# Optimization experiments

Measured on AMD Instinct MI355X. Metric: run time of the kernel, lower is better.

Reference implementation:

```python
import jax, jax.numpy as jnp
import numpy as np

B, S, D_IN, D_H, D_LAT, D_OUT = 128, 1024, 64, 256, 256, 128
N_PIECES = 20
NEG_BIG = -99999.0


def setup_inputs() -> dict:
    key = jax.random.key(0)
    ks = jax.random.split(key, 12)
    def lin(k, fan_in, fan_out):
        bound = 1.0 / np.sqrt(fan_in)
        kw, kb = jax.random.split(k)
        w = jax.random.uniform(kw, (fan_in, fan_out), minval=-bound, maxval=bound, dtype=jnp.float32)
        b = jax.random.uniform(kb, (fan_out,), minval=-bound, maxval=bound, dtype=jnp.float32)
        return w, b
    x = jax.random.normal(ks[0], (B, S, D_IN), dtype=jnp.float32)
    mask = jax.random.randint(ks[1], (B, S, 1), 0, 2, dtype=jnp.int32)
    phi_w1, phi_b1 = lin(ks[2], D_IN, D_H)
    phi_w2, phi_b2 = lin(ks[3], D_H, D_LAT)
    rho_w1, rho_b1 = lin(ks[4], D_LAT, D_H)
    rho_w2, rho_b2 = lin(ks[5], D_H, D_OUT)
    pool_w = 0.1 * jax.random.normal(ks[6], (D_LAT, N_PIECES + 1), dtype=jnp.float32)
    return dict(x=x, mask=mask, phi_w1=phi_w1, phi_b1=phi_b1, phi_w2=phi_w2, phi_b2=phi_b2,
                rho_w1=rho_w1, rho_b1=rho_b1, rho_w2=rho_w2, rho_b2=rho_b2, pool_w=pool_w)


def _fspool(x, n, w):
    # x: [B, C, S] features per channel over set dim; n: [B] ragged sizes; w: [C, P+1]
    b, c, s = x.shape
    # positions mapped to [0,1] ratio of the (n-1)-long valid prefix (fill_sizes)
    ratio = jnp.arange(s, dtype=jnp.float32)[None, :] / jnp.maximum(n.astype(jnp.float32) - 1.0, 1.0)[:, None]  # [B,S]
    m = (ratio <= 1.0).astype(x.dtype)          # [B,S], first n positions valid
    ratio = jnp.minimum(ratio, 1.0)
    # piecewise-linear interpolation of continuous weight function (determine_weight)
    pos = N_PIECES * ratio                       # [B,S]
    idx = jnp.floor(pos).astype(jnp.int32)
    frac = (pos - idx)[:, None, :]               # [B,1,S]
    left = jnp.take(w, idx, axis=1).transpose(1, 0, 2)                                   # [B,C,S]
    right = jnp.take(w, jnp.clip(idx + 1, 0, N_PIECES), axis=1).transpose(1, 0, 2)       # [B,C,S]
    weight = (1.0 - frac) * left + frac * right  # [B,C,S]
    # push padded entries to the bottom, sort descending per channel
    xm = x + (1.0 - m)[:, None, :] * NEG_BIG
    xs = jnp.flip(jnp.sort(xm, axis=2), axis=2)  # descending
    return jnp.sum(xs * weight * m[:, None, :], axis=2)  # [B,C]


def reference(x, mask, phi_w1, phi_b1, phi_w2, phi_b2, rho_w1, rho_b1, rho_w2, rho_b2, pool_w):
    # phi per-element MLP: [B,S,d_in] -> [B,S,d_lat]
    h = jax.nn.relu(jnp.einsum('bsi,ih->bsh', x, phi_w1) + phi_b1)
    feat = jnp.einsum('bsh,hl->bsl', h, phi_w2) + phi_b2
    feat = jnp.transpose(feat, (0, 2, 1))        # [B, d_lat, S]
    n = jnp.sum(mask, axis=1).squeeze(-1)        # [B]
    pooled = _fspool(feat, n, pool_w)            # [B, d_lat]
    # rho MLP
    h2 = jax.nn.relu(pooled @ rho_w1 + rho_b1)
    return h2 @ rho_w2 + rho_b2                  # [B, d_out]
```

## Files before the change

### kernel.cpp

```cpp
#include <hip/hip_runtime.h>
#include <hip/hip_bf16.h>

#define B_    128
#define S_    1024
#define DIN   64
#define DH    256
#define DLAT  256
#define DOUT  128
#define NPIECES 20

typedef short bf16x8 __attribute__((ext_vector_type(8)));
typedef float f32x4  __attribute__((ext_vector_type(4)));
typedef unsigned short u16x2 __attribute__((ext_vector_type(2)));

__device__ __forceinline__ unsigned short f2b(float f) {
    union { float f; unsigned u; } a; a.f = f;
    unsigned r = a.u + 0x7fffu + ((a.u >> 16) & 1u);
    return (unsigned short)(r >> 16);
}
__device__ __forceinline__ float b2f_u(unsigned u16bits) {
    union { unsigned u; float f; } a; a.u = u16bits << 16;
    return a.f;
}
__device__ __forceinline__ unsigned pmaxu(unsigned a, unsigned b) {
    union { unsigned u; u16x2 v; } A, Bv, R;
    A.u = a; Bv.u = b;
    R.v = __builtin_elementwise_max(A.v, Bv.v);
    return R.u;
}
__device__ __forceinline__ unsigned pminu(unsigned a, unsigned b) {
    union { unsigned u; u16x2 v; } A, Bv, R;
    A.u = a; Bv.u = b;
    R.v = __builtin_elementwise_min(A.v, Bv.v);
    return R.u;
}
__device__ __forceinline__ unsigned ror16(unsigned x) { return (x >> 16) | (x << 16); }

__device__ __forceinline__ bf16x8 cvt8(float4 a, float4 b) {
    bf16x8 o;
    o[0] = (short)f2b(a.x); o[1] = (short)f2b(a.y); o[2] = (short)f2b(a.z); o[3] = (short)f2b(a.w);
    o[4] = (short)f2b(b.x); o[5] = (short)f2b(b.y); o[6] = (short)f2b(b.z); o[7] = (short)f2b(b.w);
    return o;
}

__global__ __launch_bounds__(256) void k_prep(const int* __restrict__ mask,
                                              int* __restrict__ nv,
                                              const float* __restrict__ w1,
                                              short* __restrict__ w1pk,
                                              const float* __restrict__ w2,
                                              short* __restrict__ w2pk) {
    __shared__ int parts[4];
    const int blk = blockIdx.x, t = threadIdx.x;
    if (blk < B_) {
        int sum = 0;
        #pragma unroll
        for (int q = 0; q < S_ / 256; ++q) sum += mask[blk * S_ + q * 256 + t];
        #pragma unroll
        for (int off = 32; off > 0; off >>= 1) sum += __shfl_down(sum, off, 64);
        if ((t & 63) == 0) parts[t >> 6] = sum;
        __syncthreads();
        if (t == 0) nv[blk] = max(parts[0] + parts[1] + parts[2] + parts[3], 2);
    } else if (blk < B_ + 8) {
        int c = (blk - B_) * 256 + t;
        int l = c & 63, ks = (c >> 6) % 2, nt = (c >> 6) / 2;
        int col = nt * 16 + (l & 15);
        int k0 = ks * 32 + (l >> 4) * 8;
        bf16x8 o;
        #pragma unroll
        for (int j = 0; j < 8; ++j) o[j] = (short)f2b(w1[(size_t)(k0 + j) * DH + col]);
        *(bf16x8*)(w1pk + (size_t)c * 8) = o;
    } else {
        int c = (blk - B_ - 8) * 256 + t;
        int l = c & 63, ks = (c >> 6) % 8, nt = (c >> 6) / 8;
        int col = nt * 16 + (l & 15);
        int k0 = ks * 32 + (l >> 4) * 8;
        bf16x8 o;
        #pragma unroll
        for (int j = 0; j < 8; ++j) o[j] = (short)f2b(w2[(size_t)(k0 + j) * DLAT + col]);
        *(bf16x8*)(w2pk + (size_t)c * 8) = o;
    }
}

__global__ __launch_bounds__(256) void k_phi_mfma(const float* __restrict__ x,
                                                  const short* __restrict__ w1pk,
                                                  const short* __restrict__ w2pk,
                                                  const float* __restrict__ b1,
                                                  const float* __restrict__ b2,
                                                  const int* __restrict__ nv,
                                                  unsigned short* __restrict__ feat) {
    const int b    = blockIdx.y;
    const int tile = blockIdx.x;
    const int s0   = tile * 64;
    if (s0 >= nv[b]) return;
    const int tid  = threadIdx.x;
    const int w    = tid >> 6;
    const int lane = tid & 63;
    const int c15  = lane & 15;
    const int q    = lane >> 4;

    __shared__ __align__(16) char lds[64 * 256 * 2];

    f32x4 acc1[4][4];
    #pragma unroll
    for (int mt = 0; mt < 4; ++mt)
        #pragma unroll
        for (int nt = 0; nt < 4; ++nt) acc1[mt][nt] = (f32x4)0.f;

    const float* xb = x + ((size_t)b * S_ + s0) * DIN;
    bf16x8 a1[4][2], bw[4][2];
    #pragma unroll
    for (int mt = 0; mt < 4; ++mt)
        #pragma unroll
        for (int ks = 0; ks < 2; ++ks) {
            const float* p = xb + (size_t)(mt * 16 + c15) * DIN + ks * 32 + q * 8;
            float4 v0 = *(const float4*)p;
            float4 v1 = *(const float4*)(p + 4);
            a1[mt][ks] = cvt8(v0, v1);
        }
    #pragma unroll
    for (int nt = 0; nt < 4; ++nt)
        #pragma unroll
        for (int ks = 0; ks < 2; ++ks)
            bw[nt][ks] = *(const bf16x8*)(w1pk + ((size_t)((w * 4 + nt) * 2 + ks) * 64 + lane) * 8);
    #pragma unroll
    for (int ks = 0; ks < 2; ++ks)
        #pragma unroll
        for (int mt = 0; mt < 4; ++mt)
            #pragma unroll
            for (int nt = 0; nt < 4; ++nt)
                acc1[mt][nt] = __builtin_amdgcn_mfma_f32_16x16x32_bf16(a1[mt][ks], bw[nt][ks], acc1[mt][nt], 0, 0, 0);

    #pragma unroll
    for (int nt = 0; nt < 4; ++nt) {
        int chan = (w * 4 + nt) * 16 + c15;
        float bias = b1[chan];
        #pragma unroll
        for (int mt = 0; mt < 4; ++mt)
            #pragma unroll
            for (int r = 0; r < 4; ++r) {
                int pos = mt * 16 + q * 4 + r;
                float hv = fmaxf(acc1[mt][nt][r] + bias, 0.f);
                int byte = pos * 512 + chan * 2;
                byte ^= (pos & 7) << 4;
                *(unsigned short*)(lds + byte) = f2b(hv);
            }
    }
    __syncthreads();

    f32x4 acc2[4][4];
    #pragma unroll
    for (int mt = 0; mt < 4; ++mt)
        #pragma unroll
        for (int nt = 0; nt < 4; ++nt) acc2[mt][nt] = (f32x4)0.f;

    for (int ks2 = 0; ks2 < 8; ++ks2) {
        bf16x8 af[4];
        #pragma unroll
        for (int mt = 0; mt < 4; ++mt) {
            int pos = mt * 16 + c15;
            int byte = pos * 512 + ks2 * 64 + q * 16;
            byte ^= (pos & 7) << 4;
            af[mt] = *(const bf16x8*)(lds + byte);
        }
        #pragma unroll
        for (int nt = 0; nt < 4; ++nt) {
            bf16x8 bf_ = *(const bf16x8*)(w2pk + ((size_t)((w * 4 + nt) * 8 + ks2) * 64 + lane) * 8);
            #pragma unroll
            for (int mt = 0; mt < 4; ++mt)
                acc2[mt][nt] = __builtin_amdgcn_mfma_f32_16x16x32_bf16(af[mt], bf_, acc2[mt][nt], 0, 0, 0);
        }
    }
    __syncthreads();

    #pragma unroll
    for (int nt = 0; nt < 4; ++nt) {
        int chan = (w * 4 + nt) * 16 + c15;
        float bias = b2[chan];
        #pragma unroll
        for (int mt = 0; mt < 4; ++mt) {
            unsigned u0 = (unsigned)f2b(acc2[mt][nt][0] + bias) | ((unsigned)f2b(acc2[mt][nt][1] + bias) << 16);
            unsigned u1 = (unsigned)f2b(acc2[mt][nt][2] + bias) | ((unsigned)f2b(acc2[mt][nt][3] + bias) << 16);
            int pos0 = mt * 16 + q * 4;
            int byte = chan * 128 + pos0 * 2;
            byte ^= (chan & 7) << 4;
            *(uint2*)(lds + byte) = uint2{u0, u1};
        }
    }
    __syncthreads();

    #pragma unroll
    for (int it = 0; it < 8; ++it) {
        int L = it * 256 + tid;
        int chan = L >> 3, chunk = L & 7;
        int byte = chan * 128 + chunk * 16;
        byte ^= (chan & 7) << 4;
        uint4 val = *(const uint4*)(lds + byte);
        *(uint4*)((char*)(feat + ((size_t)b * DLAT + chan) * S_ + s0) + chunk * 16) = val;
    }
}


template <int T0, int NREGS>
__device__ __forceinline__ void loadcvt4(const unsigned short* __restrict__ fp, int i0, int n,
                                         unsigned (&r)[NREGS]) {
    uint4 a = *(const uint4*)(fp + i0);
    r[T0 + 0] = a.x; r[T0 + 1] = a.y; r[T0 + 2] = a.z; r[T0 + 3] = a.w;
    #pragma unroll
    for (int t = 0; t < 4; ++t) {
        unsigned u = r[T0 + t];
        unsigned sgn = (u >> 15) & 0x00010001u;
        unsigned key = u ^ ((sgn * 0x7FFFu) | 0x80008000u);
        int e0 = i0 + 2 * t;
        unsigned keep = (e0 + 1 < n) ? 0xFFFFFFFFu : ((e0 < n) ? 0x0000FFFFu : 0u);
        r[T0 + t] = key & keep;
    }
}

template <int T0, int NREGS>
__device__ __forceinline__ void pass_cross(unsigned (&r)[NREGS], int lane, int m, int k) {
    bool lower = ((lane & m) == 0);
    bool dz = (((lane << 3) & k) == 0);
    bool sel = (dz == lower);
    #pragma unroll
    for (int t = 0; t < 4; ++t) {
        unsigned p = __shfl_xor(r[T0 + t], m, 64);
        unsigned mx = pmaxu(r[T0 + t], p), mn = pminu(r[T0 + t], p);
        r[T0 + t] = sel ? mx : mn;
    }
}

template <int T0, int NREGS>
__device__ __forceinline__ void pass_pair(unsigned (&r)[NREGS], int lane, int jr, int k) {
    #pragma unroll
    for (int t = 0; t < 4; ++t)
        if ((t & jr) == 0) {
            int ta = T0 + t, tb = T0 + (t | jr);
            unsigned mx = pmaxu(r[ta], r[tb]), mn = pminu(r[ta], r[tb]);
            bool dz = ((((lane << 3) | (t << 1)) & k) == 0);
            r[ta] = dz ? mx : mn;
            r[tb] = dz ? mn : mx;
        }
}

template <int T0, int NREGS>
__device__ __forceinline__ void pass_inpack(unsigned (&r)[NREGS], int lane, int k) {
    #pragma unroll
    for (int t = 0; t < 4; ++t) {
        unsigned v = r[T0 + t];
        unsigned sw = ror16(v);
        unsigned mx = pmaxu(v, sw), mn = pminu(v, sw);
        bool dz = ((((lane << 3) | (t << 1)) & k) == 0);
        unsigned de = (mx & 0x0000FFFFu) | (mn & 0xFFFF0000u);
        unsigned as = (mn & 0x0000FFFFu) | (mx & 0xFFFF0000u);
        r[T0 + t] = dz ? de : as;
    }
}

template <int NET, int T0, int NREGS>
__device__ __forceinline__ void sort_net(unsigned (&r)[NREGS], int lane) {
    #pragma unroll
    for (int k = 2; k <= NET; k <<= 1) {
        #pragma unroll
        for (int j = k >> 1; j > 0; j >>= 1) {
            if (j >= 8)      pass_cross<T0>(r, lane, j >> 3, k);
            else if (j >= 2) pass_pair<T0>(r, lane, j >> 1, k);
            else             pass_inpack<T0>(r, lane, k);
        }
    }
}

__device__ __forceinline__ void merge_desc512_dual(unsigned (&r)[8], int lane) {
    #pragma unroll
    for (int j = 256; j >= 8; j >>= 1) {
        const int m = j >> 3;
        bool sel = ((lane & m) == 0);
        #pragma unroll
        for (int t = 0; t < 8; ++t) {
            unsigned p = __shfl_xor(r[t], m, 64);
            unsigned mx = pmaxu(r[t], p), mn = pminu(r[t], p);
            r[t] = sel ? mx : mn;
        }
    }
    #pragma unroll
    for (int jr = 2; jr >= 1; jr >>= 1)
        #pragma unroll
        for (int g = 0; g < 8; g += 4)
            #pragma unroll
            for (int t = 0; t < 4; ++t)
                if ((t & jr) == 0) {
                    unsigned a = r[g + t], bb = r[g + (t | jr)];
                    r[g + t]        = pmaxu(a, bb);
                    r[g + (t | jr)] = pminu(a, bb);
                }
    #pragma unroll
    for (int t = 0; t < 8; ++t) {
        unsigned sw = ror16(r[t]);
        unsigned mx = pmaxu(r[t], sw), mn = pminu(r[t], sw);
        r[t] = (mx & 0x0000FFFFu) | (mn & 0xFFFF0000u);
    }
}

template <bool FASTW, int T0, int NREGS>
__device__ __forceinline__ float wsum(const unsigned (&r)[NREGS], int rankBase, int n,
                                      float invd, const float* __restrict__ pw) {
    float acc = 0.f;
    float k0 = 0.f, k1 = 0.f, k2 = 0.f; int ib = 0;
    if (FASTW) {
        float rb = fminf((float)rankBase * invd, 1.0f);
        ib = (int)((float)NPIECES * rb);
        if (ib > NPIECES) ib = NPIECES;
        k0 = pw[ib]; k1 = pw[min(ib + 1, NPIECES)]; k2 = pw[min(ib + 2, NPIECES)];
    }
    #pragma unroll
    for (int t = 0; t < 4; ++t)
        #pragma unroll
        for (int h = 0; h < 2; ++h) {
            int i = rankBase + 2 * t + h;
            unsigned key = h ? (r[T0 + t] >> 16) : (r[T0 + t] & 0xFFFFu);
            unsigned tneg = ((key >> 15) & 1u) ^ 1u;
            unsigned u = key ^ (0x8000u | (tneg * 0x7FFFu));
            float v = (i < n) ? b2f_u(u) : 0.f;
            float ratio = fminf((float)i * invd, 1.0f);
            float pos = (float)NPIECES * ratio;
            int idx = (int)pos;
            float frac = pos - (float)idx;
            float L, R;
            if (FASTW) { L = (idx == ib) ? k0 : k1; R = (idx == ib) ? k1 : k2; }
            else       { L = pw[idx];  R = pw[min(idx + 1, NPIECES)]; }
            acc = fmaf(v, fmaf(frac, R - L, L), acc);
        }
    return acc;
}

__device__ __forceinline__ float fsp_sum16(const unsigned short* __restrict__ fp,
                                           int n, const float* __restrict__ pw, int lane) {
    const int base = lane * 16;
    unsigned r[8];
    {
        const uint4* q4 = (const uint4*)(fp + base);
        uint4 a = q4[0], bq = q4[1];
        r[0] = a.x;  r[1] = a.y;  r[2] = a.z;  r[3] = a.w;
        r[4] = bq.x; r[5] = bq.y; r[6] = bq.z; r[7] = bq.w;
    }
    #pragma unroll
    for (int t = 0; t < 8; ++t) {
        unsigned u = r[t];
        unsigned sgn = (u >> 15) & 0x00010001u;
        unsigned key = u ^ ((sgn * 0x7FFFu) | 0x80008000u);
        int i0 = base + 2 * t;
        unsigned keep = (i0 + 1 < n) ? 0xFFFFFFFFu : ((i0 < n) ? 0x0000FFFFu : 0u);
        r[t] = key & keep;
    }
    #pragma unroll
    for (int k = 2; k <= 1024; k <<= 1) {
        #pragma unroll
        for (int j = k >> 1; j > 0; j >>= 1) {
            if (j >= 16) {
                const int m = j >> 4;
                const bool dz  = (((lane * 16) & k) == 0);
                const bool sel = (dz == ((lane & m) == 0));
                #pragma unroll
                for (int t = 0; t < 8; ++t) {
                    unsigned p = __shfl_xor(r[t], m, 64);
                    unsigned mx = pmaxu(r[t], p), mn = pminu(r[t], p);
                    r[t] = sel ? mx : mn;
                }
            } else if (j >= 2) {
                const int jr = j >> 1;
                #pragma unroll
                for (int t = 0; t < 8; ++t)
                    if ((t & jr) == 0) {
                        const int tb = t | jr;
                        unsigned mx = pmaxu(r[t], r[tb]), mn = pminu(r[t], r[tb]);
                        const bool dz = ((((lane * 16) | (2 * t)) & k) == 0);
                        r[t]  = dz ? mx : mn;
                        r[tb] = dz ? mn : mx;
                    }
            } else {
                #pragma unroll
                for (int t = 0; t < 8; ++t) {
                    unsigned sw = ror16(r[t]);
                    unsigned mx = pmaxu(r[t], sw), mn = pminu(r[t], sw);
                    const bool dz = ((((lane * 16) | (2 * t)) & k) == 0);
                    unsigned de = (mx & 0x0000FFFFu) | (mn & 0xFFFF0000u);
                    unsigned as = (mn & 0x0000FFFFu) | (mx & 0xFFFF0000u);
                    r[t] = dz ? de : as;
                }
            }
        }
    }
    const float invd = 1.0f / (float)(n - 1);
    float acc = 0.f;
    float rb = fminf((float)base * invd, 1.0f);
    int ib = (int)((float)NPIECES * rb);
    if (ib > NPIECES) ib = NPIECES;
    float k0 = pw[ib], k1 = pw[min(ib + 1, NPIECES)], k2 = pw[min(ib + 2, NPIECES)];
    #pragma unroll
    for (int t = 0; t < 8; ++t)
        #pragma unroll
        for (int h = 0; h < 2; ++h) {
            int i = base + 2 * t + h;
            unsigned key = h ? (r[t] >> 16) : (r[t] & 0xFFFFu);
            unsigned tneg = ((key >> 15) & 1u) ^ 1u;
            unsigned u = key ^ (0x8000u | (tneg * 0x7FFFu));
            float v = (i < n) ? b2f_u(u) : 0.f;
            float ratio = fminf((float)i * invd, 1.0f);
            float pos = (float)NPIECES * ratio;
            int idx = (int)pos;
            float frac = pos - (float)idx;
            float L = (idx == ib) ? k0 : k1, R = (idx == ib) ? k1 : k2;
            acc = fmaf(v, fmaf(frac, R - L, L), acc);
        }
    return acc;
}

__global__ __launch_bounds__(256) void k_fspool4(const unsigned short* __restrict__ feat,
                                                 const int* __restrict__ nv,
                                                 const float* __restrict__ pool_w,
                                                 float* __restrict__ pooled) {
    const int gw   = blockIdx.x * 4 + (threadIdx.x >> 6);
    const int lane = threadIdx.x & 63;
    const int b = gw >> 8, c = gw & 255;
    const int n = nv[b];
    const unsigned short* fp = feat + ((size_t)b * DLAT + c) * S_;
    const float* pw = pool_w + c * (NPIECES + 1);
    const float invd = 1.0f / (float)(n - 1);

    float res;
    if (n <= 512) {
        unsigned r[4];
        loadcvt4<0>(fp, lane * 8, n, r);
        sort_net<512, 0>(r, lane);
        res = (n >= 141) ? wsum<true, 0>(r, lane * 8, n, invd, pw)
                         : wsum<false, 0>(r, lane * 8, n, invd, pw);
    } else if (n <= 640) {
        unsigned r[8];
        loadcvt4<0>(fp, lane * 8, n, r);
        loadcvt4<4>(fp, 512 + lane * 8, n, r);
        sort_net<512, 0>(r, lane);
        sort_net<128, 4>(r, lane);
        unsigned pa[4], pb[4];
        #pragma unroll
        for (int t = 0; t < 4; ++t) pa[t] = ror16(__shfl_xor(r[7 - t], 63, 64));
        #pragma unroll
        for (int t = 0; t < 4; ++t) pb[t] = ror16(__shfl_xor(r[3 - t], 63, 64));
        #pragma unroll
        for (int t = 0; t < 4; ++t) r[t]     = pmaxu(r[t], pa[t]);
        #pragma unroll
        for (int t = 0; t < 4; ++t) r[4 + t] = pminu(r[4 + t], pb[t]);
        merge_desc512_dual(r, lane);
        res = wsum<true, 0>(r, lane * 8, n, invd, pw)
            + wsum<true, 4>(r, 512 + lane * 8, n, invd, pw);
    } else {
        res = fsp_sum16(fp, n, pw, lane);
    }
    #pragma unroll
    for (int off = 32; off > 0; off >>= 1) res += __shfl_xor(res, off, 64);
    if (lane == 0) pooled[gw] = res;
}

__global__ __launch_bounds__(256) void k_rho(const float* __restrict__ pooled,
                                             const float* __restrict__ w1,
                                             const float* __restrict__ b1,
                                             const float* __restrict__ w2,
                                             const float* __restrict__ b2,
                                             float* __restrict__ out) {
    const int b = blockIdx.x, t = threadIdx.x;
    __shared__ float pl[DLAT];
    __shared__ float h2[DH];
    pl[t] = pooled[b * DLAT + t];
    __syncthreads();
    float acc = b1[t];
    for (int k = 0; k < DLAT; ++k) acc = fmaf(pl[k], w1[k * DH + t], acc);
    h2[t] = fmaxf(acc, 0.f);
    __syncthreads();
    if (t < DOUT) {
        float o = b2[t];
        for (int k = 0; k < DH; ++k) o = fmaf(h2[k], w2[k * DOUT + t], o);
        out[b * DOUT + t] = o;
    }
}

extern "C" void kernel_launch(void* const* d_in, const int* in_sizes, int n_in,
                              void* d_out, int out_size, void* d_ws, size_t ws_size,
                              hipStream_t stream) {
    const float* x     = (const float*)d_in[0];
    const int*   mask  = (const int*)d_in[1];
    const float* pw1   = (const float*)d_in[2];
    const float* pb1   = (const float*)d_in[3];
    const float* pw2   = (const float*)d_in[4];
    const float* pb2   = (const float*)d_in[5];
    const float* rw1   = (const float*)d_in[6];
    const float* rb1   = (const float*)d_in[7];
    const float* rw2   = (const float*)d_in[8];
    const float* rb2   = (const float*)d_in[9];
    const float* poolw = (const float*)d_in[10];
    float* out = (float*)d_out;

    char* ws = (char*)d_ws;
    size_t off = 0;
    int* nv = (int*)ws;                          off += 1024;
    short* w1pk  = (short*)(ws + off);           off += (size_t)DIN * DH * 2;
    short* w2pk  = (short*)(ws + off);           off += (size_t)DH * DLAT * 2;
    unsigned short* feat = (unsigned short*)(ws + off); off += (size_t)B_ * DLAT * S_ * 2;
    float* pooled = (float*)(ws + off);

    k_prep<<<B_ + 8 + 32, 256, 0, stream>>>(mask, nv, pw1, w1pk, pw2, w2pk);
    k_phi_mfma<<<dim3(S_ / 64, B_), 256, 0, stream>>>(x, w1pk, w2pk, pb1, pb2, nv, feat);
    k_fspool4<<<(B_ * DLAT) / 4, 256, 0, stream>>>(feat, nv, poolw, pooled);
    k_rho<<<B_, 256, 0, stream>>>(pooled, rw1, rb1, rw2, rb2, out);
}
```

Before: 132.8 us.

## Roll bitonic sort stages into loops and unify large-n path via two 512-sorts plus merge

Replaces the fully unrolled bitonic sort networks with partially rolled loops over stage k and cross-lane distance j, and hardcodes the first in-register stages. The separate 16-element-per-lane path for n>640 is removed; that case now reuses the two-half 512 sort plus dual merge. Byte-permute instructions replace the mask/or packing of min/max halves. The intent is to cut instruction-cache footprint and code size, and to share one code path across all set sizes, at the cost of loop overhead and runtime-indexed shuffles.

```diff
diff --git a/kernel.cpp b/kernel.cpp
--- a/kernel.cpp
+++ b/kernel.cpp
@@ -35,6 +35,13 @@
     return R.u;
 }
 __device__ __forceinline__ unsigned ror16(unsigned x) { return (x >> 16) | (x << 16); }
+__device__ __forceinline__ unsigned permb(unsigned a, unsigned b, unsigned s) {
+    return __builtin_amdgcn_perm(a, b, s);
+}
+__device__ __forceinline__ unsigned keycvt(unsigned u) {
+    unsigned sgn = (u >> 15) & 0x00010001u;
+    return u ^ ((sgn * 0x7FFFu) | 0x80008000u);
+}
 
 __device__ __forceinline__ bf16x8 cvt8(float4 a, float4 b) {
     bf16x8 o;
@@ -207,9 +214,7 @@
     r[T0 + 0] = a.x; r[T0 + 1] = a.y; r[T0 + 2] = a.z; r[T0 + 3] = a.w;
     #pragma unroll
     for (int t = 0; t < 4; ++t) {
-        unsigned u = r[T0 + t];
-        unsigned sgn = (u >> 15) & 0x00010001u;
-        unsigned key = u ^ ((sgn * 0x7FFFu) | 0x80008000u);
+        unsigned key = keycvt(r[T0 + t]);
         int e0 = i0 + 2 * t;
         unsigned keep = (e0 + 1 < n) ? 0xFFFFFFFFu : ((e0 < n) ? 0x0000FFFFu : 0u);
         r[T0 + t] = key & keep;
@@ -217,86 +222,95 @@
 }
 
 template <int T0, int NREGS>
-__device__ __forceinline__ void pass_cross(unsigned (&r)[NREGS], int lane, int m, int k) {
-    bool lower = ((lane & m) == 0);
-    bool dz = (((lane << 3) & k) == 0);
-    bool sel = (dz == lower);
+__device__ __forceinline__ void sort512_loop(unsigned (&r)[NREGS], int lane, int kmax) {
     #pragma unroll
     for (int t = 0; t < 4; ++t) {
-        unsigned p = __shfl_xor(r[T0 + t], m, 64);
-        unsigned mx = pmaxu(r[T0 + t], p), mn = pminu(r[T0 + t], p);
-        r[T0 + t] = sel ? mx : mn;
-    }
-}
-
-template <int T0, int NREGS>
-__device__ __forceinline__ void pass_pair(unsigned (&r)[NREGS], int lane, int jr, int k) {
-    #pragma unroll
-    for (int t = 0; t < 4; ++t)
-        if ((t & jr) == 0) {
-            int ta = T0 + t, tb = T0 + (t | jr);
-            unsigned mx = pmaxu(r[ta], r[tb]), mn = pminu(r[ta], r[tb]);
-            bool dz = ((((lane << 3) | (t << 1)) & k) == 0);
-            r[ta] = dz ? mx : mn;
-            r[tb] = dz ? mn : mx;
-        }
-}
-
-template <int T0, int NREGS>
-__device__ __forceinline__ void pass_inpack(unsigned (&r)[NREGS], int lane, int k) {
+        unsigned v = r[T0 + t], sw = ror16(v);
+        unsigned mx = pmaxu(v, sw), mn = pminu(v, sw);
+        r[T0 + t] = ((t & 1) == 0) ? permb(mn, mx, 0x07060100u) : permb(mx, mn, 0x07060100u);
+    }
+    {
+        unsigned mx0 = pmaxu(r[T0 + 0], r[T0 + 1]), mn0 = pminu(r[T0 + 0], r[T0 + 1]);
+        r[T0 + 0] = mx0; r[T0 + 1] = mn0;
+        unsigned mx1 = pmaxu(r[T0 + 2], r[T0 + 3]), mn1 = pminu(r[T0 + 2], r[T0 + 3]);
+        r[T0 + 2] = mn1; r[T0 + 3] = mx1;
+    }
     #pragma unroll
     for (int t = 0; t < 4; ++t) {
-        unsigned v = r[T0 + t];
-        unsigned sw = ror16(v);
+        unsigned v = r[T0 + t], sw = ror16(v);
         unsigned mx = pmaxu(v, sw), mn = pminu(v, sw);
-        bool dz = ((((lane << 3) | (t << 1)) & k) == 0);
-        unsigned de = (mx & 0x0000FFFFu) | (mn & 0xFFFF0000u);
-        unsigned as = (mn & 0x0000FFFFu) | (mx & 0xFFFF0000u);
-        r[T0 + t] = dz ? de : as;
-    }
-}
-
-template <int NET, int T0, int NREGS>
-__device__ __forceinline__ void sort_net(unsigned (&r)[NREGS], int lane) {
-    #pragma unroll
-    for (int k = 2; k <= NET; k <<= 1) {
-        #pragma unroll
-        for (int j = k >> 1; j > 0; j >>= 1) {
-            if (j >= 8)      pass_cross<T0>(r, lane, j >> 3, k);
-            else if (j >= 2) pass_pair<T0>(r, lane, j >> 1, k);
-            else             pass_inpack<T0>(r, lane, k);
-        }
-    }
-}
-
-__device__ __forceinline__ void merge_desc512_dual(unsigned (&r)[8], int lane) {
-    #pragma unroll
+        r[T0 + t] = (t < 2) ? permb(mn, mx, 0x07060100u) : permb(mx, mn, 0x07060100u);
+    }
+    #pragma clang loop unroll(disable)
+    for (int k = 8; k <= kmax; k <<= 1) {
+        const bool dzk = (((lane << 3) & k) == 0);
+        #pragma clang loop unroll(disable)
+        for (int j = k >> 1; j >= 8; j >>= 1) {
+            const int m = j >> 3;
+            const bool sel = (dzk == ((lane & m) == 0));
+            #pragma unroll
+            for (int t = 0; t < 4; ++t) {
+                unsigned p = (unsigned)__shfl_xor((int)r[T0 + t], m, 64);
+                unsigned mx = pmaxu(r[T0 + t], p), mn = pminu(r[T0 + t], p);
+                r[T0 + t] = sel ? mx : mn;
+            }
+        }
+        #pragma unroll
+        for (int t = 0; t < 2; ++t) {
+            unsigned a = r[T0 + t], bb = r[T0 + t + 2];
+            unsigned mx = pmaxu(a, bb), mn = pminu(a, bb);
+            r[T0 + t]     = dzk ? mx : mn;
+            r[T0 + t + 2] = dzk ? mn : mx;
+        }
+        #pragma unroll
+        for (int t = 0; t < 4; t += 2) {
+            unsigned a = r[T0 + t], bb = r[T0 + t + 1];
+            unsigned mx = pmaxu(a, bb), mn = pminu(a, bb);
+            r[T0 + t]     = dzk ? mx : mn;
+            r[T0 + t + 1] = dzk ? mn : mx;
+        }
+        #pragma unroll
+        for (int t = 0; t < 4; ++t) {
+            unsigned v = r[T0 + t], sw = ror16(v);
+            unsigned mx = pmaxu(v, sw), mn = pminu(v, sw);
+            unsigned de = permb(mn, mx, 0x07060100u);
+            unsigned as = permb(mx, mn, 0x07060100u);
+            r[T0 + t] = dzk ? de : as;
+        }
+    }
+}
+
+__device__ __forceinline__ void merge512_dual_loop(unsigned (&r)[8], int lane) {
+    #pragma clang loop unroll(disable)
     for (int j = 256; j >= 8; j >>= 1) {
         const int m = j >> 3;
-        bool sel = ((lane & m) == 0);
+        const bool sel = ((lane & m) == 0);
         #pragma unroll
         for (int t = 0; t < 8; ++t) {
-            unsigned p = __shfl_xor(r[t], m, 64);
+            unsigned p = (unsigned)__shfl_xor((int)r[t], m, 64);
             unsigned mx = pmaxu(r[t], p), mn = pminu(r[t], p);
             r[t] = sel ? mx : mn;
         }
     }
     #pragma unroll
-    for (int jr = 2; jr >= 1; jr >>= 1)
-        #pragma unroll
-        for (int g = 0; g < 8; g += 4)
-            #pragma unroll
-            for (int t = 0; t < 4; ++t)
-                if ((t & jr) == 0) {
-                    unsigned a = r[g + t], bb = r[g + (t | jr)];
-                    r[g + t]        = pmaxu(a, bb);
-                    r[g + (t | jr)] = pminu(a, bb);
-                }
+    for (int g = 0; g < 8; g += 4) {
+        #pragma unroll
+        for (int t = 0; t < 2; ++t) {
+            unsigned a = r[g + t], bb = r[g + t + 2];
+            r[g + t]     = pmaxu(a, bb);
+            r[g + t + 2] = pminu(a, bb);
+        }
+        #pragma unroll
+        for (int t = 0; t < 4; t += 2) {
+            unsigned a = r[g + t], bb = r[g + t + 1];
+            r[g + t]     = pmaxu(a, bb);
+            r[g + t + 1] = pminu(a, bb);
+        }
+    }
     #pragma unroll
     for (int t = 0; t < 8; ++t) {
         unsigned sw = ror16(r[t]);
-        unsigned mx = pmaxu(r[t], sw), mn = pminu(r[t], sw);
-        r[t] = (mx & 0x0000FFFFu) | (mn & 0xFFFF0000u);
+        r[t] = permb(pminu(r[t], sw), pmaxu(r[t], sw), 0x07060100u);
     }
 }
 
@@ -332,92 +346,10 @@
     return acc;
 }
 
-__device__ __forceinline__ float fsp_sum16(const unsigned short* __restrict__ fp,
-                                           int n, const float* __restrict__ pw, int lane) {
-    const int base = lane * 16;
-    unsigned r[8];
-    {
-        const uint4* q4 = (const uint4*)(fp + base);
-        uint4 a = q4[0], bq = q4[1];
-        r[0] = a.x;  r[1] = a.y;  r[2] = a.z;  r[3] = a.w;
-        r[4] = bq.x; r[5] = bq.y; r[6] = bq.z; r[7] = bq.w;
-    }
-    #pragma unroll
-    for (int t = 0; t < 8; ++t) {
-        unsigned u = r[t];
-        unsigned sgn = (u >> 15) & 0x00010001u;
-        unsigned key = u ^ ((sgn * 0x7FFFu) | 0x80008000u);
-        int i0 = base + 2 * t;
-        unsigned keep = (i0 + 1 < n) ? 0xFFFFFFFFu : ((i0 < n) ? 0x0000FFFFu : 0u);
-        r[t] = key & keep;
-    }
-    #pragma unroll
-    for (int k = 2; k <= 1024; k <<= 1) {
-        #pragma unroll
-        for (int j = k >> 1; j > 0; j >>= 1) {
-            if (j >= 16) {
-                const int m = j >> 4;
-                const bool dz  = (((lane * 16) & k) == 0);
-                const bool sel = (dz == ((lane & m) == 0));
-                #pragma unroll
-                for (int t = 0; t < 8; ++t) {
-                    unsigned p = __shfl_xor(r[t], m, 64);
-                    unsigned mx = pmaxu(r[t], p), mn = pminu(r[t], p);
-                    r[t] = sel ? mx : mn;
-                }
-            } else if (j >= 2) {
-                const int jr = j >> 1;
-                #pragma unroll
-                for (int t = 0; t < 8; ++t)
-                    if ((t & jr) == 0) {
-                        const int tb = t | jr;
-                        unsigned mx = pmaxu(r[t], r[tb]), mn = pminu(r[t], r[tb]);
-                        const bool dz = ((((lane * 16) | (2 * t)) & k) == 0);
-                        r[t]  = dz ? mx : mn;
-                        r[tb] = dz ? mn : mx;
-                    }
-            } else {
-                #pragma unroll
-                for (int t = 0; t < 8; ++t) {
-                    unsigned sw = ror16(r[t]);
-                    unsigned mx = pmaxu(r[t], sw), mn = pminu(r[t], sw);
-                    const bool dz = ((((lane * 16) | (2 * t)) & k) == 0);
-                    unsigned de = (mx & 0x0000FFFFu) | (mn & 0xFFFF0000u);
-                    unsigned as = (mn & 0x0000FFFFu) | (mx & 0xFFFF0000u);
-                    r[t] = dz ? de : as;
-                }
-            }
-        }
-    }
-    const float invd = 1.0f / (float)(n - 1);
-    float acc = 0.f;
-    float rb = fminf((float)base * invd, 1.0f);
-    int ib = (int)((float)NPIECES * rb);
-    if (ib > NPIECES) ib = NPIECES;
-    float k0 = pw[ib], k1 = pw[min(ib + 1, NPIECES)], k2 = pw[min(ib + 2, NPIECES)];
-    #pragma unroll
-    for (int t = 0; t < 8; ++t)
-        #pragma unroll
-        for (int h = 0; h < 2; ++h) {
-            int i = base + 2 * t + h;
-            unsigned key = h ? (r[t] >> 16) : (r[t] & 0xFFFFu);
-            unsigned tneg = ((key >> 15) & 1u) ^ 1u;
-            unsigned u = key ^ (0x8000u | (tneg * 0x7FFFu));
-            float v = (i < n) ? b2f_u(u) : 0.f;
-            float ratio = fminf((float)i * invd, 1.0f);
-            float pos = (float)NPIECES * ratio;
-            int idx = (int)pos;
-            float frac = pos - (float)idx;
-            float L = (idx == ib) ? k0 : k1, R = (idx == ib) ? k1 : k2;
-            acc = fmaf(v, fmaf(frac, R - L, L), acc);
-        }
-    return acc;
-}
-
-__global__ __launch_bounds__(256) void k_fspool4(const unsigned short* __restrict__ feat,
-                                                 const int* __restrict__ nv,
-                                                 const float* __restrict__ pool_w,
-                                                 float* __restrict__ pooled) {
+__global__ __launch_bounds__(256) void k_fspool11(const unsigned short* __restrict__ feat,
+                                                  const int* __restrict__ nv,
+                                                  const float* __restrict__ pool_w,
+                                                  float* __restrict__ pooled) {
     const int gw   = blockIdx.x * 4 + (threadIdx.x >> 6);
     const int lane = threadIdx.x & 63;
     const int b = gw >> 8, c = gw & 255;
@@ -430,15 +362,15 @@
     if (n <= 512) {
         unsigned r[4];
         loadcvt4<0>(fp, lane * 8, n, r);
-        sort_net<512, 0>(r, lane);
+        sort512_loop<0>(r, lane, 512);
         res = (n >= 141) ? wsum<true, 0>(r, lane * 8, n, invd, pw)
                          : wsum<false, 0>(r, lane * 8, n, invd, pw);
-    } else if (n <= 640) {
+    } else {
         unsigned r[8];
         loadcvt4<0>(fp, lane * 8, n, r);
         loadcvt4<4>(fp, 512 + lane * 8, n, r);
-        sort_net<512, 0>(r, lane);
-        sort_net<128, 4>(r, lane);
+        sort512_loop<0>(r, lane, 512);
+        sort512_loop<4>(r, lane, (n <= 640) ? 128 : 512);
         unsigned pa[4], pb[4];
         #pragma unroll
         for (int t = 0; t < 4; ++t) pa[t] = ror16(__shfl_xor(r[7 - t], 63, 64));
@@ -448,11 +380,9 @@
         for (int t = 0; t < 4; ++t) r[t]     = pmaxu(r[t], pa[t]);
         #pragma unroll
         for (int t = 0; t < 4; ++t) r[4 + t] = pminu(r[4 + t], pb[t]);
-        merge_desc512_dual(r, lane);
+        merge512_dual_loop(r, lane);
         res = wsum<true, 0>(r, lane * 8, n, invd, pw)
             + wsum<true, 4>(r, 512 + lane * 8, n, invd, pw);
-    } else {
-        res = fsp_sum16(fp, n, pw, lane);
     }
     #pragma unroll
     for (int off = 32; off > 0; off >>= 1) res += __shfl_xor(res, off, 64);
@@ -507,6 +437,6 @@
 
     k_prep<<<B_ + 8 + 32, 256, 0, stream>>>(mask, nv, pw1, w1pk, pw2, w2pk);
     k_phi_mfma<<<dim3(S_ / 64, B_), 256, 0, stream>>>(x, w1pk, w2pk, pb1, pb2, nv, feat);
-    k_fspool4<<<(B_ * DLAT) / 4, 256, 0, stream>>>(feat, nv, poolw, pooled);
+    k_fspool11<<<(B_ * DLAT) / 4, 256, 0, stream>>>(feat, nv, poolw, pooled);
     k_rho<<<B_, 256, 0, stream>>>(pooled, rw1, rb1, rw2, rb2, out);
 }
```

New measurement: 143.1 us. +7.8%, slower.
